# Optimization experiments

Measured on AMD Instinct MI355X. Metric: run time of the kernel, lower is better.

Reference implementation:

```python
import jax, jax.numpy as jnp
import numpy as np

B, C, H, W = 8, 32, 256, 448


def setup_inputs() -> dict:
    key = jax.random.key(0)
    k1, k2 = jax.random.split(key)
    input1 = jax.random.normal(k1, (B, C, H, W), dtype=jnp.float32)
    input2 = jax.random.normal(k2, (B, 2, H, W), dtype=jnp.float32)  # flow (u, v)
    return {"input1": input1, "input2": input2, "kernel_size": 1}


def _forward_splat(input1, input2):
    """Forward warp: splat each source pixel to (x+u, y+v) with bilinear weights,
    accumulating via scatter-add (kernel_size=1 -> 2x2 bilinear footprint)."""
    b, c, h, w = input1.shape
    u = input2[:, 0]  # [B,H,W] horizontal flow
    v = input2[:, 1]  # [B,H,W] vertical flow
    xs = jnp.arange(w, dtype=input2.dtype)
    ys = jnp.arange(h, dtype=input2.dtype)
    tx = xs[None, None, :] + u  # target x, [B,H,W]
    ty = ys[None, :, None] + v  # target y, [B,H,W]
    x0 = jnp.floor(tx).astype(jnp.int32)
    y0 = jnp.floor(ty).astype(jnp.int32)
    fx = tx - x0.astype(tx.dtype)
    fy = ty - y0.astype(ty.dtype)

    vals = input1.transpose(0, 2, 3, 1).reshape(b * h * w, c)  # [BHW, C]
    out = jnp.zeros((b * h * w, c), dtype=input1.dtype)
    batch_off = (jnp.arange(b, dtype=jnp.int32) * (h * w))[:, None, None]

    for dx, dy in ((0, 0), (1, 0), (0, 1), (1, 1)):
        xx = x0 + dx
        yy = y0 + dy
        wx = fx if dx == 1 else (1.0 - fx)
        wy = fy if dy == 1 else (1.0 - fy)
        wgt = wx * wy  # [B,H,W]
        valid = (xx >= 0) & (xx < w) & (yy >= 0) & (yy < h)
        wgt = jnp.where(valid, wgt, 0.0)
        idx = batch_off + jnp.clip(yy, 0, h - 1) * w + jnp.clip(xx, 0, w - 1)
        out = out.at[idx.reshape(-1)].add(wgt.reshape(-1, 1) * vals)

    return out.reshape(b, h, w, c).transpose(0, 3, 1, 2)


def reference(input1, input2, kernel_size):
    # kernel_size=1 corresponds to the standard bilinear (2x2) splat footprint.
    return _forward_splat(input1, input2)
```

## Files before the change

kernel.cpp:

```cpp
#include <hip/hip_runtime.h>
#include <hip/hip_fp16.h>

constexpr int B = 8;
constexpr int C = 32;
constexpr int H = 256;
constexpr int W = 448;
constexpr int HW = H * W;

constexpr int TW  = 64;
constexpr int TH  = 8;
constexpr int RAD = 3;
constexpr int WXV = 72;
constexpr int WY  = TH + 2 * RAD;
constexpr int NV  = WXV * WY;
constexpr int NT  = 512;
constexpr int GITER = (NV + NT - 1) / NT;
constexpr int NG4 = (WXV / 4) * WY;
constexpr int NITEM = NG4 * 8;
constexpr int KITER = (NITEM + NT - 1) / NT;

static __device__ __forceinline__ unsigned pkrtz(float a, float b) {
    return __builtin_bit_cast(unsigned, __builtin_amdgcn_cvt_pkrtz(a, b));
}

static __device__ __forceinline__ __half2 h2(unsigned u) {
    union { unsigned u; __half2 h; } x;
    x.u = u;
    return x.h;
}

__global__ __launch_bounds__(NT)
void splat_out(const float* __restrict__ in1,
               const float* __restrict__ flow,
               float* __restrict__ out,
               unsigned* __restrict__ wcnt,
               unsigned* __restrict__ wlist,
               unsigned cap) {
    __shared__ unsigned long long mAllS[NT];
    __shared__ unsigned long long mDxS[NT];
    __shared__ unsigned long long mDyS[NT];
    __shared__ uint2    geomW[NV];
    __shared__ unsigned valV[8 * NV];

    int bid = blockIdx.x;
    int b = bid & 7;
    int t = bid >> 3;
    int ty = t / 7;
    int tx = t - ty * 7;
    int ox = tx * TW, oy = ty * TH;
    int tid = threadIdx.x;
    int qlx = tid & 63, qly = tid >> 6;
    int qx = ox + qlx, qy = oy + qly;

    mAllS[tid] = 0ull;
    mDxS[tid]  = 0ull;
    mDyS[tid]  = 0ull;
    __syncthreads();

    const int fbase = b * 2 * HW;
#pragma unroll
    for (int k = 0; k < GITER; ++k) {
        int i = tid + k * NT;
        if (i < NV) {
            int wy = i / WXV, wv = i - wy * WXV;
            int gx = ox + wv - 4;
            int sy = oy + wy - RAD;
            uint2 wd = make_uint2(0u, 0u);
            if ((unsigned)gx < (unsigned)W && (unsigned)sy < (unsigned)H) {
                int g = sy * W + gx;
                float u = flow[fbase + g];
                float v = flow[fbase + g + HW];
                float txf = (float)gx + u;
                float tyf = (float)sy + v;
                float x0f = floorf(txf), y0f = floorf(tyf);
                int rx = (int)x0f - gx, ry = (int)y0f - sy;
                if (rx >= -RAD && rx <= RAD - 1 && ry >= -RAD && ry <= RAD - 1) {
                    float fx = txf - x0f, fy = tyf - y0f;
                    wd.x = pkrtz((1.f - fx) * (1.f - fy), fx * (1.f - fy));
                    wd.y = pkrtz((1.f - fx) * fy,         fx * fy);
#pragma unroll
                    for (int corner = 0; corner < 4; ++corner) {
                        int dxx = corner & 1, dyy = corner >> 1;
                        int ccx = gx + rx + dxx - ox;
                        int ccy = sy + ry + dyy - oy;
                        if ((unsigned)ccx < (unsigned)TW &&
                            (unsigned)ccy < (unsigned)TH) {
                            int cell = ccy * TW + ccx;
                            unsigned long long bit =
                                1ull << ((3 - (ry + dyy)) * 8 + (3 - (rx + dxx)));
                            atomicOr(&mAllS[cell], bit);
                            if (dxx) atomicOr(&mDxS[cell], bit);
                            if (dyy) atomicOr(&mDyS[cell], bit);
                        }
                    }
                } else if (wv >= 4 && wv < 4 + TW &&
                           wy >= RAD && wy < RAD + TH) {
                    unsigned slot = atomicAdd(wcnt, 1u);
                    if (slot < cap) wlist[slot] = ((unsigned)b << 17) | (unsigned)g;
                }
            }
            geomW[i] = wd;
        }
    }

    const float* inb = in1 + (size_t)b * C * HW;

    auto stage = [&](int pass) {
#pragma unroll
        for (int k = 0; k < KITER; ++k) {
            int id = tid + k * NT;
            if (id < NITEM) {
                int g4 = id % NG4;
                int cp = id / NG4;
                int wy = g4 / (WXV / 4);
                int wv4 = (g4 - wy * (WXV / 4)) * 4;
                int row = min(max(oy + wy - RAD, 0), H - 1);
                int gxb = min(max(ox + wv4 - 4, 0), W - 4);
                const float* base = inb + (size_t)(16 * pass + 2 * cp) * HW
                                        + (size_t)row * W + gxb;
                float4 a = *reinterpret_cast<const float4*>(base);
                float4 c = *reinterpret_cast<const float4*>(base + (size_t)HW);
                uint4 wv_;
                wv_.x = pkrtz(a.x, c.x);
                wv_.y = pkrtz(a.y, c.y);
                wv_.z = pkrtz(a.z, c.z);
                wv_.w = pkrtz(a.w, c.w);
                *reinterpret_cast<uint4*>(&valV[cp * NV + wy * WXV + wv4]) = wv_;
            }
        }
    };

    stage(0);
    __syncthreads();

    const unsigned long long m0  = mAllS[tid];
    const unsigned long long mdx = mDxS[tid];
    const unsigned long long mdy = mDyS[tid];
    const int qbase = (qly + RAD) * WXV + (qlx + 4);
    float* outp = out + (size_t)b * C * HW + qy * W + qx;

    auto gather = [&](float* o) {
        __half2 acc2[8];
#pragma unroll
        for (int k = 0; k < 8; ++k) acc2[k] = h2(0u);
        unsigned long long m = m0;
        while (m) {
            int j = (int)__builtin_ctzll(m);
            m &= m - 1;
            int wi = qbase + ((j >> 3) - 3) * WXV + ((j & 7) - 3);
            unsigned dxx = (unsigned)(mdx >> j) & 1u;
            unsigned dyy = (unsigned)(mdy >> j) & 1u;
            uint2 wd2 = geomW[wi];
            unsigned wd = dyy ? wd2.y : wd2.x;
            unsigned hq = (wd >> (16u * dxx)) & 0xFFFFu;
            __half2 w2 = h2(hq | (hq << 16));
            acc2[0] = __hfma2(h2(valV[0 * NV + wi]), w2, acc2[0]);
            acc2[1] = __hfma2(h2(valV[1 * NV + wi]), w2, acc2[1]);
            acc2[2] = __hfma2(h2(valV[2 * NV + wi]), w2, acc2[2]);
            acc2[3] = __hfma2(h2(valV[3 * NV + wi]), w2, acc2[3]);
            acc2[4] = __hfma2(h2(valV[4 * NV + wi]), w2, acc2[4]);
            acc2[5] = __hfma2(h2(valV[5 * NV + wi]), w2, acc2[5]);
            acc2[6] = __hfma2(h2(valV[6 * NV + wi]), w2, acc2[6]);
            acc2[7] = __hfma2(h2(valV[7 * NV + wi]), w2, acc2[7]);
        }
#pragma unroll
        for (int k = 0; k < 8; ++k) {
            float2 f = __half22float2(acc2[k]);
            o[(size_t)(2 * k) * HW]     = f.x;
            o[(size_t)(2 * k + 1) * HW] = f.y;
        }
    };

    gather(outp);
    __syncthreads();
    stage(1);
    __syncthreads();
    gather(outp + (size_t)16 * HW);
}

__global__ void outlier_combined(const float* __restrict__ in1,
                                 const float* __restrict__ flow,
                                 float* __restrict__ out,
                                 const unsigned* __restrict__ wcnt,
                                 const unsigned* __restrict__ wlist,
                                 unsigned cap) {
    unsigned n = *wcnt;
    if (n <= cap) {
        unsigned total = n * 8u;
        for (unsigned idx = blockIdx.x * blockDim.x + threadIdx.x;
             idx < total; idx += gridDim.x * blockDim.x) {
            unsigned e = wlist[idx >> 3];
            int c0 = (int)(idx & 7u) * 4;
            int bb = (int)(e >> 17);
            int p  = (int)(e & 0x1FFFFu);
            int y = p / W, x = p - y * W;

            float u = flow[(bb * 2 + 0) * HW + p];
            float v = flow[(bb * 2 + 1) * HW + p];
            float txf = (float)x + u;
            float tyf = (float)y + v;
            float fx0 = floorf(txf), fy0 = floorf(tyf);
            int x0 = (int)fx0, y0 = (int)fy0;
            float fx = txf - fx0, fy = tyf - fy0;
            float w00 = (1.0f - fx) * (1.0f - fy);
            float w10 = fx * (1.0f - fy);
            float w01 = (1.0f - fx) * fy;
            float w11 = fx * fy;
            bool vx0 = (x0 >= 0) && (x0 < W);
            bool vx1 = (x0 + 1 >= 0) && (x0 + 1 < W);
            bool vy0 = (y0 >= 0) && (y0 < H);
            bool vy1 = (y0 + 1 >= 0) && (y0 + 1 < H);
            long o00 = (long)y0 * W + x0;

            const float* src  = in1 + (size_t)bb * C * HW + (size_t)c0 * HW + p;
            float*       dstb = out + (size_t)bb * C * HW + (size_t)c0 * HW;
            for (int c = 0; c < 4; ++c) {
                float val = src[(size_t)c * HW];
                float* ob = dstb + (size_t)c * HW;
                if (vx0 && vy0) atomicAdd(ob + o00,         w00 * val);
                if (vx1 && vy0) atomicAdd(ob + o00 + 1,     w10 * val);
                if (vx0 && vy1) atomicAdd(ob + o00 + W,     w01 * val);
                if (vx1 && vy1) atomicAdd(ob + o00 + W + 1, w11 * val);
            }
        }
    } else {
        int npix = B * HW;
        for (int idx = blockIdx.x * blockDim.x + threadIdx.x;
             idx < npix; idx += gridDim.x * blockDim.x) {
            int b = idx / HW;
            int p = idx - b * HW;
            int y = p / W, x = p - y * W;
            float u = flow[(b * 2 + 0) * HW + p];
            float v = flow[(b * 2 + 1) * HW + p];
            float txf = (float)x + u;
            float tyf = (float)y + v;
            float fx0 = floorf(txf), fy0 = floorf(tyf);
            int x0 = (int)fx0, y0 = (int)fy0;
            int rx = x0 - x, ry = y0 - y;
            bool handled = (rx >= -RAD) && (rx <= RAD - 1) &&
                           (ry >= -RAD) && (ry <= RAD - 1);
            if (handled) continue;
            float fx = txf - fx0, fy = tyf - fy0;
            float w00 = (1.0f - fx) * (1.0f - fy);
            float w10 = fx * (1.0f - fy);
            float w01 = (1.0f - fx) * fy;
            float w11 = fx * fy;
            bool vx0 = (x0 >= 0) && (x0 < W);
            bool vx1 = (x0 + 1 >= 0) && (x0 + 1 < W);
            bool vy0 = (y0 >= 0) && (y0 < H);
            bool vy1 = (y0 + 1 >= 0) && (y0 + 1 < H);
            long o00 = (long)y0 * W + x0;
            const float* src = in1 + (size_t)b * C * HW + p;
            float* dstb = out + (size_t)b * C * HW;
            for (int c = 0; c < C; ++c) {
                float val = src[(size_t)c * HW];
                float* ob = dstb + (size_t)c * HW;
                if (vx0 && vy0) atomicAdd(ob + o00,         w00 * val);
                if (vx1 && vy0) atomicAdd(ob + o00 + 1,     w10 * val);
                if (vx0 && vy1) atomicAdd(ob + o00 + W,     w01 * val);
                if (vx1 && vy1) atomicAdd(ob + o00 + W + 1, w11 * val);
            }
        }
    }
}

extern "C" void kernel_launch(void* const* d_in, const int* in_sizes, int n_in,
                              void* d_out, int out_size, void* d_ws, size_t ws_size,
                              hipStream_t stream) {
    const float* in1  = (const float*)d_in[0];
    const float* flow = (const float*)d_in[1];
    float* out = (float*)d_out;

    unsigned* wcnt  = (unsigned*)d_ws;
    unsigned* wlist = wcnt + 4;
    unsigned cap = 0;
    if (ws_size >= 64) {
        size_t c = ws_size / sizeof(unsigned) - 4;
        cap = (c > 0x7FFFFFFFull) ? 0x7FFFFFFFu : (unsigned)c;
    }

    hipMemsetAsync(wcnt, 0, sizeof(unsigned), stream);

    int nblocks = B * (H / TH) * (W / TW);
    splat_out<<<nblocks, NT, 0, stream>>>(in1, flow, out, wcnt, wlist, cap);

    outlier_combined<<<256, 256, 0, stream>>>(in1, flow, out, wcnt, wlist, cap);
}
```

Measured before the change: 112.6 us.

## Stage all 32 channels in one pass and derive corner offsets from geometry

Stages all 32 channels into shared memory as packed fp16 quads in a single pass, instead of two 16-channel passes. The neighbour-mask walk and its shared-memory reads now run once instead of twice, and two barriers go away. The separate dx/dy bitmask arrays and their atomics are replaced by a per-source byte holding the splat offset, from which each gather recomputes the corner. Shared memory per block grows by roughly half, which may reduce how many blocks fit per CU.

Result: faster. 108.4 us (-3.8%).

```diff
diff --git a/kernel.cpp b/kernel.cpp
--- a/kernel.cpp
+++ b/kernel.cpp
@@ -37,10 +37,9 @@
                unsigned* __restrict__ wlist,
                unsigned cap) {
     __shared__ unsigned long long mAllS[NT];
-    __shared__ unsigned long long mDxS[NT];
-    __shared__ unsigned long long mDyS[NT];
-    __shared__ uint2    geomW[NV];
-    __shared__ unsigned valV[8 * NV];
+    __shared__ unsigned char     geomR8[NV];
+    __shared__ uint2             geomW[NV];
+    __shared__ __align__(16) uint2 valV2[8 * NV];
 
     int bid = blockIdx.x;
     int b = bid & 7;
@@ -53,8 +52,6 @@
     int qx = ox + qlx, qy = oy + qly;
 
     mAllS[tid] = 0ull;
-    mDxS[tid]  = 0ull;
-    mDyS[tid]  = 0ull;
     __syncthreads();
 
     const int fbase = b * 2 * HW;
@@ -66,6 +63,7 @@
             int gx = ox + wv - 4;
             int sy = oy + wy - RAD;
             uint2 wd = make_uint2(0u, 0u);
+            unsigned gr = 0xFFu;
             if ((unsigned)gx < (unsigned)W && (unsigned)sy < (unsigned)H) {
                 int g = sy * W + gx;
                 float u = flow[fbase + g];
@@ -78,6 +76,7 @@
                     float fx = txf - x0f, fy = tyf - y0f;
                     wd.x = pkrtz((1.f - fx) * (1.f - fy), fx * (1.f - fy));
                     wd.y = pkrtz((1.f - fx) * fy,         fx * fy);
+                    gr = (unsigned)(rx + RAD) | ((unsigned)(ry + RAD) << 3);
 #pragma unroll
                     for (int corner = 0; corner < 4; ++corner) {
                         int dxx = corner & 1, dyy = corner >> 1;
@@ -89,8 +88,6 @@
                             unsigned long long bit =
                                 1ull << ((3 - (ry + dyy)) * 8 + (3 - (rx + dxx)));
                             atomicOr(&mAllS[cell], bit);
-                            if (dxx) atomicOr(&mDxS[cell], bit);
-                            if (dyy) atomicOr(&mDyS[cell], bit);
                         }
                     }
                 } else if (wv >= 4 && wv < 4 + TW &&
@@ -99,83 +96,78 @@
                     if (slot < cap) wlist[slot] = ((unsigned)b << 17) | (unsigned)g;
                 }
             }
-            geomW[i] = wd;
+            geomR8[i] = (unsigned char)gr;
+            geomW[i]  = wd;
         }
     }
 
     const float* inb = in1 + (size_t)b * C * HW;
-
-    auto stage = [&](int pass) {
-#pragma unroll
-        for (int k = 0; k < KITER; ++k) {
-            int id = tid + k * NT;
-            if (id < NITEM) {
-                int g4 = id % NG4;
-                int cp = id / NG4;
-                int wy = g4 / (WXV / 4);
-                int wv4 = (g4 - wy * (WXV / 4)) * 4;
-                int row = min(max(oy + wy - RAD, 0), H - 1);
-                int gxb = min(max(ox + wv4 - 4, 0), W - 4);
-                const float* base = inb + (size_t)(16 * pass + 2 * cp) * HW
-                                        + (size_t)row * W + gxb;
-                float4 a = *reinterpret_cast<const float4*>(base);
-                float4 c = *reinterpret_cast<const float4*>(base + (size_t)HW);
-                uint4 wv_;
-                wv_.x = pkrtz(a.x, c.x);
-                wv_.y = pkrtz(a.y, c.y);
-                wv_.z = pkrtz(a.z, c.z);
-                wv_.w = pkrtz(a.w, c.w);
-                *reinterpret_cast<uint4*>(&valV[cp * NV + wy * WXV + wv4]) = wv_;
-            }
-        }
-    };
-
-    stage(0);
+#pragma unroll
+    for (int k = 0; k < KITER; ++k) {
+        int id = tid + k * NT;
+        if (id < NITEM) {
+            int g4 = id % NG4;
+            int pp = id / NG4;
+            int wy = g4 / (WXV / 4);
+            int wv4 = (g4 - wy * (WXV / 4)) * 4;
+            int row = min(max(oy + wy - RAD, 0), H - 1);
+            int gxb = min(max(ox + wv4 - 4, 0), W - 4);
+            const float* base = inb + (size_t)(4 * pp) * HW
+                                    + (size_t)row * W + gxb;
+            float4 c0 = *reinterpret_cast<const float4*>(base);
+            float4 c1 = *reinterpret_cast<const float4*>(base + (size_t)HW);
+            float4 c2 = *reinterpret_cast<const float4*>(base + (size_t)2 * HW);
+            float4 c3 = *reinterpret_cast<const float4*>(base + (size_t)3 * HW);
+            int vbase = pp * NV + wy * WXV + wv4;
+            uint4* dst = reinterpret_cast<uint4*>(&valV2[vbase]);
+            uint4 w0, w1;
+            w0.x = pkrtz(c0.x, c1.x); w0.y = pkrtz(c2.x, c3.x);
+            w0.z = pkrtz(c0.y, c1.y); w0.w = pkrtz(c2.y, c3.y);
+            w1.x = pkrtz(c0.z, c1.z); w1.y = pkrtz(c2.z, c3.z);
+            w1.z = pkrtz(c0.w, c1.w); w1.w = pkrtz(c2.w, c3.w);
+            dst[0] = w0;
+            dst[1] = w1;
+        }
+    }
     __syncthreads();
 
-    const unsigned long long m0  = mAllS[tid];
-    const unsigned long long mdx = mDxS[tid];
-    const unsigned long long mdy = mDyS[tid];
+    const unsigned long long m0 = mAllS[tid];
     const int qbase = (qly + RAD) * WXV + (qlx + 4);
     float* outp = out + (size_t)b * C * HW + qy * W + qx;
 
-    auto gather = [&](float* o) {
-        __half2 acc2[8];
-#pragma unroll
-        for (int k = 0; k < 8; ++k) acc2[k] = h2(0u);
-        unsigned long long m = m0;
-        while (m) {
-            int j = (int)__builtin_ctzll(m);
-            m &= m - 1;
-            int wi = qbase + ((j >> 3) - 3) * WXV + ((j & 7) - 3);
-            unsigned dxx = (unsigned)(mdx >> j) & 1u;
-            unsigned dyy = (unsigned)(mdy >> j) & 1u;
-            uint2 wd2 = geomW[wi];
-            unsigned wd = dyy ? wd2.y : wd2.x;
-            unsigned hq = (wd >> (16u * dxx)) & 0xFFFFu;
-            __half2 w2 = h2(hq | (hq << 16));
-            acc2[0] = __hfma2(h2(valV[0 * NV + wi]), w2, acc2[0]);
-            acc2[1] = __hfma2(h2(valV[1 * NV + wi]), w2, acc2[1]);
-            acc2[2] = __hfma2(h2(valV[2 * NV + wi]), w2, acc2[2]);
-            acc2[3] = __hfma2(h2(valV[3 * NV + wi]), w2, acc2[3]);
-            acc2[4] = __hfma2(h2(valV[4 * NV + wi]), w2, acc2[4]);
-            acc2[5] = __hfma2(h2(valV[5 * NV + wi]), w2, acc2[5]);
-            acc2[6] = __hfma2(h2(valV[6 * NV + wi]), w2, acc2[6]);
-            acc2[7] = __hfma2(h2(valV[7 * NV + wi]), w2, acc2[7]);
-        }
-#pragma unroll
-        for (int k = 0; k < 8; ++k) {
-            float2 f = __half22float2(acc2[k]);
-            o[(size_t)(2 * k) * HW]     = f.x;
-            o[(size_t)(2 * k + 1) * HW] = f.y;
-        }
-    };
-
-    gather(outp);
-    __syncthreads();
-    stage(1);
-    __syncthreads();
-    gather(outp + (size_t)16 * HW);
+    __half2 acc2[16];
+#pragma unroll
+    for (int k = 0; k < 16; ++k) acc2[k] = h2(0u);
+
+    unsigned long long m = m0;
+    while (m) {
+        int j = (int)__builtin_ctzll(m);
+        m &= m - 1;
+        int wi = qbase + ((j >> 3) - 3) * WXV + ((j & 7) - 3);
+        unsigned g8 = geomR8[wi];
+        unsigned dxx = 6u - (unsigned)(j & 7) - (g8 & 7u);
+        unsigned dyy = 6u - (unsigned)(j >> 3) - (g8 >> 3);
+        uint2 wd2 = geomW[wi];
+        unsigned wd = dyy ? wd2.y : wd2.x;
+        unsigned hq = (wd >> (16u * dxx)) & 0xFFFFu;
+        __half2 w2 = h2(hq | (hq << 16));
+#pragma unroll
+        for (int pp = 0; pp < 8; ++pp) {
+            uint2 vv = valV2[pp * NV + wi];
+            acc2[2 * pp + 0] = __hfma2(h2(vv.x), w2, acc2[2 * pp + 0]);
+            acc2[2 * pp + 1] = __hfma2(h2(vv.y), w2, acc2[2 * pp + 1]);
+        }
+    }
+
+#pragma unroll
+    for (int pp = 0; pp < 8; ++pp) {
+        float2 f01 = __half22float2(acc2[2 * pp + 0]);
+        float2 f23 = __half22float2(acc2[2 * pp + 1]);
+        outp[(size_t)(4 * pp + 0) * HW] = f01.x;
+        outp[(size_t)(4 * pp + 1) * HW] = f01.y;
+        outp[(size_t)(4 * pp + 2) * HW] = f23.x;
+        outp[(size_t)(4 * pp + 3) * HW] = f23.y;
+    }
 }
 
 __global__ void outlier_combined(const float* __restrict__ in1,
```
